# Optimization experiments

Hardware: AMD Instinct MI355X
Metric: run time of the kernel (lower is better)

The kernel has to match this reference:

```python
import jax, jax.numpy as jnp
import numpy as np

B, S, E, H, D, R = 2, 2048, 1024, 16, 64, 16


def setup_inputs() -> dict:
    key = jax.random.key(0)
    ks = jax.random.split(key, 9)
    s = lambda k, shape, fan: jax.random.normal(k, shape, dtype=jnp.float32) / np.sqrt(fan)
    return {
        "x": jax.random.normal(ks[0], (B, S, E), dtype=jnp.float32),
        "Wq": s(ks[1], (H, E, D), E),
        "bq": jnp.zeros((H, D), jnp.float32),
        "Wk": s(ks[2], (H, E, D), E),
        "bk": jnp.zeros((H, D), jnp.float32),
        "Wvd": s(ks[3], (H, E, R), E),
        "bvd": jnp.zeros((H, R), jnp.float32),
        "Wvu": s(ks[4], (H, R, D), R),
        "bvu": jnp.zeros((H, D), jnp.float32),
    }


def reference(x, Wq, bq, Wk, bk, Wvd, bvd, Wvu, bvu):
    b, s, e = x.shape
    # per-head projections, vectorized over heads h
    q = jnp.einsum('bse,hed->bhsd', x, Wq) + bq[None, :, None, :]
    k = jnp.einsum('bse,hed->bhsd', x, Wk) + bk[None, :, None, :]
    # NOTE: original scales by sqrt(embedding_dimension), not head dim
    scores = jnp.einsum('bhsd,bhtd->bhst', q, k) / jnp.sqrt(jnp.float32(e))
    # original mask: masked_fill where key_idx < query_idx (anti-causal)
    qi = jnp.arange(s)[:, None]
    ki = jnp.arange(s)[None, :]
    scores = jnp.where(ki < qi, -jnp.inf, scores)
    att = jax.nn.softmax(scores, axis=-1)  # dropout p=0 (eval)
    # low-rank value: up(down(x))
    vd = jnp.einsum('bse,her->bhsr', x, Wvd) + bvd[None, :, None, :]
    v = jnp.einsum('bhsr,hrd->bhsd', vd, Wvu) + bvu[None, :, None, :]
    out = jnp.einsum('bhst,bhtd->bhsd', att, v)
    # concat heads along last dim (head order = stack order)
    return out.transpose(0, 2, 1, 3).reshape(b, s, -1)
```

## Files before the change

kernel.cpp:

```cpp
#include <hip/hip_runtime.h>
#include <stdint.h>

#define B_ 2
#define S_ 2048
#define E_ 1024
#define H_ 16
#define D_ 64
#define R_ 16

typedef short s16x8 __attribute__((ext_vector_type(8)));
typedef float f32x4 __attribute__((ext_vector_type(4)));

#define K1_ 0.045084220027780106f
#define K0_ -28.853900817779268f

__device__ __forceinline__ unsigned short f2bf(float f) {
  union { float f; unsigned u; } v; v.f = f;
  return (unsigned short)((v.u + 0x8000u) >> 16);
}

__device__ __forceinline__ void load_lds16(const void* g, void* l) {
  __builtin_amdgcn_global_load_lds(
      (__attribute__((address_space(1))) void*)(g),
      (__attribute__((address_space(3))) void*)(l), 16, 0, 0);
}

__global__ void k_prep(const float* __restrict__ x,
                       const float* __restrict__ Wq, const float* __restrict__ Wk,
                       const float* __restrict__ Wvd, const float* __restrict__ Wvu,
                       const float* __restrict__ bq, const float* __restrict__ bk,
                       const float* __restrict__ bvd, const float* __restrict__ bvu,
                       unsigned short* __restrict__ xb, unsigned short* __restrict__ Wt,
                       float* __restrict__ ball) {
  __shared__ float T[64][65];
  const int blk = blockIdx.x;
  const int t = threadIdx.x;
  if (blk < 4096) {
    int i = (blk * 256 + t) * 4;
    float4 v = *(const float4*)(x + i);
    ushort4 o;
    o.x = f2bf(v.x); o.y = f2bf(v.y); o.z = f2bf(v.z); o.w = f2bf(v.w);
    *(ushort4*)(xb + i) = o;
  } else if (blk < 4608) {
    const int bb = blk - 4096;
    const int which = bb >> 8;
    const int h = (bb >> 4) & 15;
    const int et = bb & 15;
    const float scl = which ? 1.f : K1_;
    const float* src = (which ? Wk : Wq) + (h * E_ + et * 64) * D_;
#pragma unroll
    for (int pr = 0; pr < 4; ++pr) {
      const int row = pr * 16 + (t >> 4);
      const int col = (t & 15) * 4;
      float4 v = *(const float4*)(src + row * 64 + col);
      T[row][col] = v.x; T[row][col + 1] = v.y; T[row][col + 2] = v.z; T[row][col + 3] = v.w;
    }
    __syncthreads();
#pragma unroll
    for (int pr = 0; pr < 4; ++pr) {
      const int d = pr * 16 + (t >> 4);
      const int ec = (t & 15) * 4;
      ushort4 o;
      o.x = f2bf(T[ec][d] * scl); o.y = f2bf(T[ec + 1][d] * scl);
      o.z = f2bf(T[ec + 2][d] * scl); o.w = f2bf(T[ec + 3][d] * scl);
      *(ushort4*)(Wt + ((which << 10) + h * 64 + d) * 1024 + et * 64 + ec) = o;
    }
  } else if (blk < 8704) {
    const int idx = (blk - 4608) * 256 + t;
    const int row = idx >> 10;
    const int e = idx & 1023;
    const int h = row >> 6, d = row & 63;
    const float4* wd4 = (const float4*)(Wvd + (h << 14) + e * 16);
    const float* wu = Wvu + h * R_ * D_ + d;
    float acc = 0.f;
#pragma unroll
    for (int r4 = 0; r4 < 4; ++r4) {
      float4 a = wd4[r4];
      acc += a.x * wu[(r4 * 4 + 0) * 64];
      acc += a.y * wu[(r4 * 4 + 1) * 64];
      acc += a.z * wu[(r4 * 4 + 2) * 64];
      acc += a.w * wu[(r4 * 4 + 3) * 64];
    }
    Wt[(2048 + row) * 1024 + e] = f2bf(acc);
  } else {
    int n = (blk - 8704) * 256 + t;
    int which = n >> 10;
    int hd = n & 1023;
    int h = hd >> 6, d = hd & 63;
    float v;
    if (which == 0) v = bq[hd] * K1_;
    else if (which == 1) v = bk[hd];
    else {
      v = bvu[hd];
#pragma unroll
      for (int r = 0; r < R_; ++r) v += bvd[h * R_ + r] * Wvu[(h * R_ + r) * D_ + d];
    }
    ball[n] = v;
  }
}


__global__ __launch_bounds__(256, 2) void k_gemm_qkv(
    const unsigned short* __restrict__ X, const unsigned short* __restrict__ Wt,
    const float* __restrict__ ball,
    unsigned short* __restrict__ Qb, unsigned short* __restrict__ Kb,
    unsigned short* __restrict__ Vb) {
  __shared__ unsigned short As[128 * 32];
  __shared__ unsigned short Bs[128 * 32];
  const int tid = threadIdx.x;
  const int lane = tid & 63, wave = tid >> 6;
  const int quad = lane >> 4, l16 = lane & 15;
  const int mBase = blockIdx.y * 128, nBase = blockIdx.x * 128;
  const int wm = (wave & 1) * 64, wn = (wave >> 1) * 64;
  const int lrow = lane >> 2, lcol = (lane & 3) * 8;

  f32x4 acc[4][4];
#pragma unroll
  for (int mi = 0; mi < 4; ++mi)
#pragma unroll
    for (int ni = 0; ni < 4; ++ni) acc[mi][ni] = (f32x4){0.f, 0.f, 0.f, 0.f};

  for (int k0 = 0; k0 < E_; k0 += 32) {
#pragma unroll
    for (int i = 0; i < 2; ++i) {
      const int r0 = __builtin_amdgcn_readfirstlane((wave + i * 4) * 16);
      load_lds16(X + (mBase + r0 + lrow) * E_ + k0 + lcol, &As[r0 * 32]);
      load_lds16(Wt + (nBase + r0 + lrow) * E_ + k0 + lcol, &Bs[r0 * 32]);
    }
    __syncthreads();
    s16x8 af[4], bfr[4];
#pragma unroll
    for (int mi = 0; mi < 4; ++mi)
      af[mi] = *(const s16x8*)&As[(wm + mi * 16 + l16) * 32 + quad * 8];
#pragma unroll
    for (int ni = 0; ni < 4; ++ni)
      bfr[ni] = *(const s16x8*)&Bs[(wn + ni * 16 + l16) * 32 + quad * 8];
#pragma unroll
    for (int mi = 0; mi < 4; ++mi)
#pragma unroll
      for (int ni = 0; ni < 4; ++ni)
        acc[mi][ni] = __builtin_amdgcn_mfma_f32_16x16x32_bf16(af[mi], bfr[ni], acc[mi][ni], 0, 0, 0);
    __syncthreads();
  }

  const int which = nBase >> 10;
#pragma unroll
  for (int ni = 0; ni < 4; ++ni) {
    const int n = nBase + wn + ni * 16 + l16;
    const int nh = n & 1023;
    const int h = nh >> 6, d = nh & 63;
    const float bias = ball[n];
#pragma unroll
    for (int mi = 0; mi < 4; ++mi) {
      const int m0 = mBase + wm + mi * 16 + quad * 4;
      const int b = m0 >> 11;
      const int s = m0 & 2047;
      const int bh = b * H_ + h;
      if (which == 2) {
        ushort4 pk;
        pk.x = f2bf(acc[mi][ni][0] + bias);
        pk.y = f2bf(acc[mi][ni][1] + bias);
        pk.z = f2bf(acc[mi][ni][2] + bias);
        pk.w = f2bf(acc[mi][ni][3] + bias);
        *(ushort4*)(Vb + (bh * D_ + d) * S_ + s) = pk;
      } else {
        unsigned short* dst = (which == 0 ? Qb : Kb) + (bh * S_ + s) * D_ + d;
#pragma unroll
        for (int r = 0; r < 4; ++r) dst[r * D_] = f2bf(acc[mi][ni][r] + bias);
      }
    }
  }
}


__global__ __launch_bounds__(256, 4) void k_attn(
    const unsigned short* __restrict__ Qb, const unsigned short* __restrict__ Kb,
    const unsigned short* __restrict__ Vb, float* __restrict__ out) {
  __shared__ unsigned short Ks[2][2 * 64 * 32];
  __shared__ unsigned short Vs[2][2 * 64 * 32];
  __shared__ unsigned short Ps[4][16][40];
  const int tid = threadIdx.x;
  const int lane = tid & 63, wave = tid >> 6;
  const int quad = lane >> 4, l16 = lane & 15;
  const int chunk = blockIdx.x >> 8;
  const int j = blockIdx.x & 255;
  int qt = j >> 3;
  if (chunk & 1) qt = 31 - qt;
  const int bh = (j & 7) + 8 * chunk;
  const int q0 = qt * 64;
  const int lrow = lane >> 2, lcol = (lane & 3) * 8;
  const int r0 = __builtin_amdgcn_readfirstlane(wave * 16);
  const f32x4 kvec = {K0_, K0_, K0_, K0_};

  s16x8 qf[2];
  {
    const unsigned short* qp = Qb + (bh * S_ + q0 + wave * 16 + l16) * D_ + quad * 8;
    qf[0] = *(const s16x8*)qp;
    qf[1] = *(const s16x8*)(qp + 32);
  }
  f32x4 o[4];
#pragma unroll
  for (int dc = 0; dc < 4; ++dc) o[dc] = (f32x4){0.f, 0.f, 0.f, 0.f};
  float l_acc[4] = {0.f, 0.f, 0.f, 0.f};

#define DMA_KV(kt_, b_)                                                          \
  {                                                                              \
    _Pragma("unroll")                                                            \
    for (int hdc = 0; hdc < 2; ++hdc) {                                          \
      load_lds16(Kb + (bh * S_ + (kt_) * 64 + r0 + lrow) * D_ + hdc * 32 + lcol, \
                 &Ks[b_][hdc * 2048 + r0 * 32]);                                 \
      load_lds16(Vb + (bh * D_ + r0 + lrow) * S_ + (kt_) * 64 + hdc * 32 + lcol, \
                 &Vs[b_][hdc * 2048 + r0 * 32]);                                 \
    }                                                                            \
  }

  DMA_KV(qt, 0);

  int buf = 0;
  for (int kt = qt; kt < S_ / 64; ++kt) {
    __syncthreads();
    if (kt + 1 < S_ / 64) DMA_KV(kt + 1, buf ^ 1);

    const bool diag = (kt == qt);
#pragma unroll
    for (int kc = 0; kc < 2; ++kc) {
#pragma unroll
      for (int tcc = 0; tcc < 2; ++tcc) {
        const int tc = kc * 2 + tcc;
        f32x4 a = __builtin_amdgcn_mfma_f32_16x16x32_bf16(
            qf[0], *(const s16x8*)&Ks[buf][(tc * 16 + l16) * 32 + quad * 8], kvec, 0, 0, 0);
        f32x4 sc = __builtin_amdgcn_mfma_f32_16x16x32_bf16(
            qf[1], *(const s16x8*)&Ks[buf][2048 + (tc * 16 + l16) * 32 + quad * 8], a, 0, 0, 0);
        if (diag) {
#pragma unroll
          for (int r = 0; r < 4; ++r) {
            const int t = tc * 16 + l16;
            const int q = wave * 16 + quad * 4 + r;
            if (t < q) sc[r] = -200.f;
          }
        }
#pragma unroll
        for (int r = 0; r < 4; ++r) {
          float p = exp2f(sc[r]);
          l_acc[r] += p;
          Ps[wave][quad * 4 + r][tcc * 16 + l16] =
              (unsigned short)(__float_as_uint(p) >> 16);
        }
      }
      s16x8 pf = *(const s16x8*)&Ps[wave][l16][quad * 8];
#pragma unroll
      for (int dc = 0; dc < 4; ++dc) {
        s16x8 vb = *(const s16x8*)&Vs[buf][kc * 2048 + (dc * 16 + l16) * 32 + quad * 8];
        o[dc] = __builtin_amdgcn_mfma_f32_16x16x32_bf16(pf, vb, o[dc], 0, 0, 0);
      }
    }
    buf ^= 1;
  }
#undef DMA_KV

#pragma unroll
  for (int off = 1; off < 16; off <<= 1)
#pragma unroll
    for (int r = 0; r < 4; ++r) l_acc[r] += __shfl_xor(l_acc[r], off);
  float rinv[4];
#pragma unroll
  for (int r = 0; r < 4; ++r) rinv[r] = 1.f / l_acc[r];

  const int b = bh >> 4, h = bh & 15;
#pragma unroll
  for (int dc = 0; dc < 4; ++dc)
#pragma unroll
    for (int r = 0; r < 4; ++r) {
      const int s = q0 + wave * 16 + quad * 4 + r;
      out[(b * S_ + s) * (H_ * D_) + h * D_ + dc * 16 + l16] = o[dc][r] * rinv[r];
    }
}


extern "C" void kernel_launch(void* const* d_in, const int* in_sizes, int n_in,
                              void* d_out, int out_size, void* d_ws, size_t ws_size,
                              hipStream_t stream) {
  const float* x   = (const float*)d_in[0];
  const float* Wq  = (const float*)d_in[1];
  const float* bq  = (const float*)d_in[2];
  const float* Wk  = (const float*)d_in[3];
  const float* bk  = (const float*)d_in[4];
  const float* Wvd = (const float*)d_in[5];
  const float* bvd = (const float*)d_in[6];
  const float* Wvu = (const float*)d_in[7];
  const float* bvu = (const float*)d_in[8];
  float* out = (float*)d_out;

  char* ws = (char*)d_ws;
  unsigned short* xb   = (unsigned short*)(ws);
  unsigned short* Wt   = (unsigned short*)(ws + (8u << 20));
  float*          ball = (float*)(ws + (14u << 20));
  unsigned short* Qb   = (unsigned short*)(ws + (15u << 20));
  unsigned short* Kb   = (unsigned short*)(ws + (23u << 20));
  unsigned short* Vb   = (unsigned short*)(ws + (31u << 20));

  k_prep<<<8716, 256, 0, stream>>>(x, Wq, Wk, Wvd, Wvu, bq, bk, bvd, bvu, xb, Wt, ball);
  k_gemm_qkv<<<dim3(3072 / 128, 4096 / 128), 256, 0, stream>>>(xb, Wt, ball, Qb, Kb, Vb);
  k_attn<<<1024, 256, 0, stream>>>(Qb, Kb, Vb, out);
}
```

Baseline: 170.2 us.

## Balance anti-causal attention work with split-KV segments and combine kernel

Replaces the per-query-tile attention kernel with a load-balanced version: the 528 (q-tile, k-tile) pairs per head are split evenly across 32 blocks (16 or 17 steps each), and each block writes partial unnormalized outputs and row sums per segment. A new combine kernel sums the partials and normalizes. It also applies an XOR swizzle to the LDS layout of K/V to reduce bank conflicts. The cost is extra global traffic for the partials, a second kernel launch, and a dependence on enough workspace; otherwise it falls back to the old kernel.

```diff
diff --git a/kernel.cpp b/kernel.cpp
--- a/kernel.cpp
+++ b/kernel.cpp
@@ -99,7 +99,6 @@
   }
 }
 
-
 __global__ __launch_bounds__(256, 2) void k_gemm_qkv(
     const unsigned short* __restrict__ X, const unsigned short* __restrict__ Wt,
     const float* __restrict__ ball,
@@ -172,8 +171,177 @@
   }
 }
 
-
-__global__ __launch_bounds__(256, 4) void k_attn(
+__global__ __launch_bounds__(256, 4) void k_attn_bal(
+    const unsigned short* __restrict__ Qb, const unsigned short* __restrict__ Kb,
+    const unsigned short* __restrict__ Vb,
+    float* __restrict__ opart, float* __restrict__ lpart) {
+  __shared__ unsigned short Ks[2][2 * 64 * 32];
+  __shared__ unsigned short Vs[2][2 * 64 * 32];
+  __shared__ unsigned short Ps[4][16][40];
+  const int tid = threadIdx.x;
+  const int lane = tid & 63, wave = tid >> 6;
+  const int quad = lane >> 4, l16 = lane & 15;
+  const int blk = blockIdx.x;
+  const int bh = (blk & 7) + 8 * (blk >> 8);
+  const int w = (blk & 255) >> 3;
+  const int lo = (w < 16) ? 17 * w : 272 + 16 * (w - 16);
+  const int nsteps = (w < 16) ? 17 : 16;
+  const int r0 = __builtin_amdgcn_readfirstlane(wave * 16);
+  const f32x4 kvec = {K0_, K0_, K0_, K0_};
+
+  const int lrow = lane >> 2;
+  const int q3w  = ((lrow & 1) << 2) | (lane & 3);
+  const int q3e  = q3w ^ ((lrow >> 1) & 7);
+  const int sr16 = (lrow & ~1) | (q3e >> 2);
+  const int sc   = (q3e & 3) * 8;
+  const int rbase = (l16 >> 1) * 64 + ((((l16 & 1) << 2) | quad) ^ ((l16 >> 1) & 7)) * 8;
+
+  int qt = 0, uq = 0;
+  while (uq + (32 - qt) <= lo) { uq += 32 - qt; ++qt; }
+  int kt = qt + (lo - uq);
+
+  s16x8 qf0, qf1;
+  {
+    const unsigned short* qp = Qb + (bh * S_ + qt * 64 + wave * 16 + l16) * D_ + quad * 8;
+    qf0 = *(const s16x8*)qp; qf1 = *(const s16x8*)(qp + 32);
+  }
+  f32x4 o[4];
+#pragma unroll
+  for (int dc = 0; dc < 4; ++dc) o[dc] = (f32x4){0.f, 0.f, 0.f, 0.f};
+  float l_acc[4] = {0.f, 0.f, 0.f, 0.f};
+
+#define DMA_KV_B(kt_, b_)                                                         \
+  {                                                                               \
+    _Pragma("unroll")                                                             \
+    for (int hdc = 0; hdc < 2; ++hdc) {                                           \
+      load_lds16(Kb + (bh * S_ + (kt_) * 64 + r0 + sr16) * D_ + hdc * 32 + sc,    \
+                 &Ks[b_][hdc * 2048 + r0 * 32]);                                  \
+      load_lds16(Vb + (bh * D_ + r0 + sr16) * S_ + (kt_) * 64 + hdc * 32 + sc,    \
+                 &Vs[b_][hdc * 2048 + r0 * 32]);                                  \
+    }                                                                             \
+  }
+
+  DMA_KV_B(kt, 0);
+  int buf = 0;
+  int qt_n = qt, kt_n = kt;
+
+  for (int step = 0; step < nsteps; ++step) {
+    __syncthreads();
+    if (step + 1 < nsteps) {
+      if (kt_n < 31) ++kt_n; else { ++qt_n; kt_n = qt_n; }
+      DMA_KV_B(kt_n, buf ^ 1);
+    }
+
+    const bool diag = (kt == qt);
+#pragma unroll
+    for (int kc = 0; kc < 2; ++kc) {
+#pragma unroll
+      for (int tcc = 0; tcc < 2; ++tcc) {
+        const int tc = kc * 2 + tcc;
+        f32x4 a = __builtin_amdgcn_mfma_f32_16x16x32_bf16(
+            qf0, *(const s16x8*)&Ks[buf][tc * 512 + rbase], kvec, 0, 0, 0);
+        f32x4 sc4 = __builtin_amdgcn_mfma_f32_16x16x32_bf16(
+            qf1, *(const s16x8*)&Ks[buf][2048 + tc * 512 + rbase], a, 0, 0, 0);
+        if (diag) {
+#pragma unroll
+          for (int r = 0; r < 4; ++r) {
+            const int t = tc * 16 + l16;
+            const int q = wave * 16 + quad * 4 + r;
+            if (t < q) sc4[r] = -200.f;
+          }
+        }
+#pragma unroll
+        for (int r = 0; r < 4; ++r) {
+          float p = exp2f(sc4[r]);
+          l_acc[r] += p;
+          Ps[wave][quad * 4 + r][tcc * 16 + l16] =
+              (unsigned short)(__float_as_uint(p) >> 16);
+        }
+      }
+      s16x8 pf = *(const s16x8*)&Ps[wave][l16][quad * 8];
+#pragma unroll
+      for (int dc = 0; dc < 4; ++dc) {
+        s16x8 vb = *(const s16x8*)&Vs[buf][kc * 2048 + dc * 512 + rbase];
+        o[dc] = __builtin_amdgcn_mfma_f32_16x16x32_bf16(pf, vb, o[dc], 0, 0, 0);
+      }
+    }
+    buf ^= 1;
+
+    const bool segend = (kt == 31) || (step == nsteps - 1);
+    if (segend) {
+      float lr[4];
+#pragma unroll
+      for (int r = 0; r < 4; ++r) {
+        float v = l_acc[r];
+        v += __shfl_xor(v, 1); v += __shfl_xor(v, 2);
+        v += __shfl_xor(v, 4); v += __shfl_xor(v, 8);
+        lr[r] = v;
+      }
+      const int sidx = (uq < 272) ? (uq / 17) : 16 + ((uq - 272) >> 4);
+      const int slot = w - sidx;
+      const int pb = (bh * 32 + qt) * 3 + slot;
+      float* op = opart + pb * 4096 + (wave * 16) * 64;
+#pragma unroll
+      for (int dc = 0; dc < 4; ++dc)
+#pragma unroll
+        for (int r = 0; r < 4; ++r)
+          op[(quad * 4 + r) * 64 + dc * 16 + l16] = o[dc][r];
+      if (l16 == 0) {
+#pragma unroll
+        for (int r = 0; r < 4; ++r)
+          lpart[pb * 64 + wave * 16 + quad * 4 + r] = lr[r];
+      }
+      if (step + 1 < nsteps) {
+        uq += 32 - qt;
+        qt = qt_n;
+        const unsigned short* qp =
+            Qb + (bh * S_ + qt * 64 + wave * 16 + l16) * D_ + quad * 8;
+        qf0 = *(const s16x8*)qp; qf1 = *(const s16x8*)(qp + 32);
+#pragma unroll
+        for (int dc = 0; dc < 4; ++dc) o[dc] = (f32x4){0.f, 0.f, 0.f, 0.f};
+#pragma unroll
+        for (int r = 0; r < 4; ++r) l_acc[r] = 0.f;
+      }
+    }
+    kt = kt_n;
+  }
+#undef DMA_KV_B
+}
+
+__global__ void k_comb(const float* __restrict__ opart, const float* __restrict__ lpart,
+                       float* __restrict__ out) {
+  const int bh = blockIdx.x >> 5, qt = blockIdx.x & 31;
+  const int off = 32 * qt - (qt * (qt - 1)) / 2;
+  const int last = off + (32 - qt) - 1;
+  const int s0 = (off < 272) ? off / 17 : 16 + (off - 272) / 16;
+  const int s1 = (last < 272) ? last / 17 : 16 + (last - 272) / 16;
+  const int n = s1 - s0 + 1;
+  const int t = threadIdx.x;
+  const int row = t >> 2, d0 = (t & 3) * 16;
+  const int base = (bh * 32 + qt) * 3;
+  float l = 0.f;
+  f32x4 acc[4];
+#pragma unroll
+  for (int j = 0; j < 4; ++j) acc[j] = (f32x4){0.f, 0.f, 0.f, 0.f};
+  for (int s = 0; s < n; ++s) {
+    l += lpart[(base + s) * 64 + row];
+    const f32x4* op = (const f32x4*)(opart + (base + s) * 4096 + row * 64 + d0);
+#pragma unroll
+    for (int j = 0; j < 4; ++j) acc[j] += op[j];
+  }
+  const float rinv = 1.f / l;
+  const int b = bh >> 4, h = bh & 15;
+  float4* dst = (float4*)(out + (b * S_ + qt * 64 + row) * (H_ * D_) + h * D_ + d0);
+#pragma unroll
+  for (int j = 0; j < 4; ++j) {
+    float4 v;
+    v.x = acc[j][0] * rinv; v.y = acc[j][1] * rinv;
+    v.z = acc[j][2] * rinv; v.w = acc[j][3] * rinv;
+    dst[j] = v;
+  }
+}
+
+__global__ __launch_bounds__(256, 4) void k_attn_r0(
     const unsigned short* __restrict__ Qb, const unsigned short* __restrict__ Kb,
     const unsigned short* __restrict__ Vb, float* __restrict__ out) {
   __shared__ unsigned short Ks[2][2 * 64 * 32];
@@ -203,7 +371,7 @@
   for (int dc = 0; dc < 4; ++dc) o[dc] = (f32x4){0.f, 0.f, 0.f, 0.f};
   float l_acc[4] = {0.f, 0.f, 0.f, 0.f};
 
-#define DMA_KV(kt_, b_)                                                          \
+#define DMA_KV_R(kt_, b_)                                                        \
   {                                                                              \
     _Pragma("unroll")                                                            \
     for (int hdc = 0; hdc < 2; ++hdc) {                                          \
@@ -214,12 +382,12 @@
     }                                                                            \
   }
 
-  DMA_KV(qt, 0);
+  DMA_KV_R(qt, 0);
 
   int buf = 0;
   for (int kt = qt; kt < S_ / 64; ++kt) {
     __syncthreads();
-    if (kt + 1 < S_ / 64) DMA_KV(kt + 1, buf ^ 1);
+    if (kt + 1 < S_ / 64) DMA_KV_R(kt + 1, buf ^ 1);
 
     const bool diag = (kt == qt);
 #pragma unroll
@@ -256,7 +424,7 @@
     }
     buf ^= 1;
   }
-#undef DMA_KV
+#undef DMA_KV_R
 
 #pragma unroll
   for (int off = 1; off < 16; off <<= 1)
@@ -299,7 +467,21 @@
   unsigned short* Kb   = (unsigned short*)(ws + (23u << 20));
   unsigned short* Vb   = (unsigned short*)(ws + (31u << 20));
 
+  const size_t OPART_OFF = (size_t)40u << 20;
+  const size_t OPART_SZ  = (size_t)32 * 32 * 3 * 4096 * 4;
+  const size_t LPART_OFF = OPART_OFF + OPART_SZ;
+  const size_t LPART_SZ  = (size_t)32 * 32 * 3 * 64 * 4;
+  const size_t NEED      = LPART_OFF + LPART_SZ;
+
   k_prep<<<8716, 256, 0, stream>>>(x, Wq, Wk, Wvd, Wvu, bq, bk, bvd, bvu, xb, Wt, ball);
   k_gemm_qkv<<<dim3(3072 / 128, 4096 / 128), 256, 0, stream>>>(xb, Wt, ball, Qb, Kb, Vb);
-  k_attn<<<1024, 256, 0, stream>>>(Qb, Kb, Vb, out);
-}
+
+  if (ws_size >= NEED) {
+    float* opart = (float*)(ws + OPART_OFF);
+    float* lpart = (float*)(ws + LPART_OFF);
+    k_attn_bal<<<1024, 256, 0, stream>>>(Qb, Kb, Vb, opart, lpart);
+    k_comb<<<1024, 256, 0, stream>>>(opart, lpart, out);
+  } else {
+    k_attn_r0<<<1024, 256, 0, stream>>>(Qb, Kb, Vb, out);
+  }
+}
```

After: 184.2 us. 8.2% more time.

## Compute low-rank V via rank-16 down projection plus separate up-projection kernel

Applied to the files above, without the earlier changes.

Stops folding Wvd·Wvu into a full 1024x1024 V weight. The QKV GEMM now computes only the rank-16 down-projection, 256 columns instead of 1024, which cuts GEMM work by a quarter. A new k_vup kernel expands vd to the transposed V layout with bias. This adds a launch, an extra round trip through the vd buffer, and a second bf16 rounding of the intermediate.

```diff
diff --git a/kernel.cpp b/kernel.cpp
--- a/kernel.cpp
+++ b/kernel.cpp
@@ -18,6 +18,10 @@
   union { float f; unsigned u; } v; v.f = f;
   return (unsigned short)((v.u + 0x8000u) >> 16);
 }
+__device__ __forceinline__ float bf2f(unsigned short b) {
+  union { unsigned u; float f; } v; v.u = ((unsigned)b) << 16;
+  return v.f;
+}
 
 __device__ __forceinline__ void load_lds16(const void* g, void* l) {
   __builtin_amdgcn_global_load_lds(
@@ -27,9 +31,9 @@
 
 __global__ void k_prep(const float* __restrict__ x,
                        const float* __restrict__ Wq, const float* __restrict__ Wk,
-                       const float* __restrict__ Wvd, const float* __restrict__ Wvu,
+                       const float* __restrict__ Wvd,
                        const float* __restrict__ bq, const float* __restrict__ bk,
-                       const float* __restrict__ bvd, const float* __restrict__ bvu,
+                       const float* __restrict__ bvd,
                        unsigned short* __restrict__ xb, unsigned short* __restrict__ Wt,
                        float* __restrict__ ball) {
   __shared__ float T[64][65];
@@ -65,46 +69,32 @@
       o.z = f2bf(T[ec + 2][d] * scl); o.w = f2bf(T[ec + 3][d] * scl);
       *(ushort4*)(Wt + ((which << 10) + h * 64 + d) * 1024 + et * 64 + ec) = o;
     }
-  } else if (blk < 8704) {
-    const int idx = (blk - 4608) * 256 + t;
-    const int row = idx >> 10;
-    const int e = idx & 1023;
-    const int h = row >> 6, d = row & 63;
-    const float4* wd4 = (const float4*)(Wvd + (h << 14) + e * 16);
-    const float* wu = Wvu + h * R_ * D_ + d;
-    float acc = 0.f;
-#pragma unroll
-    for (int r4 = 0; r4 < 4; ++r4) {
-      float4 a = wd4[r4];
-      acc += a.x * wu[(r4 * 4 + 0) * 64];
-      acc += a.y * wu[(r4 * 4 + 1) * 64];
-      acc += a.z * wu[(r4 * 4 + 2) * 64];
-      acc += a.w * wu[(r4 * 4 + 3) * 64];
-    }
-    Wt[(2048 + row) * 1024 + e] = f2bf(acc);
+  } else if (blk < 4864) {
+    const int bb = blk - 4608;
+    const int h = bb >> 4, r = bb & 15;
+    const int e0 = t * 4;
+    const float* src = Wvd + (h << 14) + r;
+    ushort4 o;
+    o.x = f2bf(src[(e0 + 0) * 16]);
+    o.y = f2bf(src[(e0 + 1) * 16]);
+    o.z = f2bf(src[(e0 + 2) * 16]);
+    o.w = f2bf(src[(e0 + 3) * 16]);
+    *(ushort4*)(Wt + (2048 + bb) * 1024 + e0) = o;
   } else {
-    int n = (blk - 8704) * 256 + t;
+    int n = (blk - 4864) * 256 + t;
     int which = n >> 10;
     int hd = n & 1023;
-    int h = hd >> 6, d = hd & 63;
-    float v;
-    if (which == 0) v = bq[hd] * K1_;
-    else if (which == 1) v = bk[hd];
-    else {
-      v = bvu[hd];
-#pragma unroll
-      for (int r = 0; r < R_; ++r) v += bvd[h * R_ + r] * Wvu[(h * R_ + r) * D_ + d];
-    }
-    ball[n] = v;
-  }
-}
-
+    if (which == 0) ball[n] = bq[hd] * K1_;
+    else if (which == 1) ball[n] = bk[hd];
+    else if (hd < 256) ball[2048 + hd] = bvd[hd];
+  }
+}
 
 __global__ __launch_bounds__(256, 2) void k_gemm_qkv(
     const unsigned short* __restrict__ X, const unsigned short* __restrict__ Wt,
     const float* __restrict__ ball,
     unsigned short* __restrict__ Qb, unsigned short* __restrict__ Kb,
-    unsigned short* __restrict__ Vb) {
+    unsigned short* __restrict__ vd) {
   __shared__ unsigned short As[128 * 32];
   __shared__ unsigned short Bs[128 * 32];
   const int tid = threadIdx.x;
@@ -148,30 +138,62 @@
   for (int ni = 0; ni < 4; ++ni) {
     const int n = nBase + wn + ni * 16 + l16;
     const int nh = n & 1023;
-    const int h = nh >> 6, d = nh & 63;
     const float bias = ball[n];
 #pragma unroll
     for (int mi = 0; mi < 4; ++mi) {
       const int m0 = mBase + wm + mi * 16 + quad * 4;
       const int b = m0 >> 11;
       const int s = m0 & 2047;
-      const int bh = b * H_ + h;
       if (which == 2) {
-        ushort4 pk;
-        pk.x = f2bf(acc[mi][ni][0] + bias);
-        pk.y = f2bf(acc[mi][ni][1] + bias);
-        pk.z = f2bf(acc[mi][ni][2] + bias);
-        pk.w = f2bf(acc[mi][ni][3] + bias);
-        *(ushort4*)(Vb + (bh * D_ + d) * S_ + s) = pk;
+        const int h = nh >> 4, r = nh & 15;
+        const int bh = b * H_ + h;
+        unsigned short* dst = vd + (bh * S_ + s) * 16 + r;
+#pragma unroll
+        for (int rr = 0; rr < 4; ++rr) dst[rr * 16] = f2bf(acc[mi][ni][rr] + bias);
       } else {
+        const int h = nh >> 6, d = nh & 63;
+        const int bh = b * H_ + h;
         unsigned short* dst = (which == 0 ? Qb : Kb) + (bh * S_ + s) * D_ + d;
 #pragma unroll
-        for (int r = 0; r < 4; ++r) dst[r * D_] = f2bf(acc[mi][ni][r] + bias);
+        for (int rr = 0; rr < 4; ++rr) dst[rr * D_] = f2bf(acc[mi][ni][rr] + bias);
       }
     }
   }
 }
 
+__global__ __launch_bounds__(256) void k_vup(
+    const unsigned short* __restrict__ vd, const float* __restrict__ Wvu,
+    const float* __restrict__ bvu, unsigned short* __restrict__ Vb) {
+  const int blk = blockIdx.x;
+  const int bh = blk >> 6, d = blk & 63;
+  const int h = bh & 15;
+  const int s0 = threadIdx.x * 8;
+  float wu[16];
+#pragma unroll
+  for (int r = 0; r < 16; ++r) wu[r] = Wvu[(h * 16 + r) * 64 + d];
+  const float bias = bvu[h * 64 + d];
+
+  float accv[8];
+#pragma unroll
+  for (int j = 0; j < 8; ++j) accv[j] = bias;
+  const s16x8* vp = (const s16x8*)(vd + (bh * S_ + s0) * 16);
+#pragma unroll
+  for (int j = 0; j < 8; ++j) {
+    s16x8 a = vp[j * 2];
+    s16x8 b = vp[j * 2 + 1];
+#pragma unroll
+    for (int r = 0; r < 8; ++r) {
+      accv[j] += bf2f((unsigned short)a[r]) * wu[r];
+      accv[j] += bf2f((unsigned short)b[r]) * wu[8 + r];
+    }
+  }
+  ushort4 o0, o1;
+  o0.x = f2bf(accv[0]); o0.y = f2bf(accv[1]); o0.z = f2bf(accv[2]); o0.w = f2bf(accv[3]);
+  o1.x = f2bf(accv[4]); o1.y = f2bf(accv[5]); o1.z = f2bf(accv[6]); o1.w = f2bf(accv[7]);
+  unsigned short* dst = Vb + (bh * D_ + d) * S_ + s0;
+  *(ushort4*)(dst) = o0;
+  *(ushort4*)(dst + 4) = o1;
+}
 
 __global__ __launch_bounds__(256, 4) void k_attn(
     const unsigned short* __restrict__ Qb, const unsigned short* __restrict__ Kb,
@@ -298,8 +320,10 @@
   unsigned short* Qb   = (unsigned short*)(ws + (15u << 20));
   unsigned short* Kb   = (unsigned short*)(ws + (23u << 20));
   unsigned short* Vb   = (unsigned short*)(ws + (31u << 20));
-
-  k_prep<<<8716, 256, 0, stream>>>(x, Wq, Wk, Wvd, Wvu, bq, bk, bvd, bvu, xb, Wt, ball);
-  k_gemm_qkv<<<dim3(3072 / 128, 4096 / 128), 256, 0, stream>>>(xb, Wt, ball, Qb, Kb, Vb);
+  unsigned short* vd   = (unsigned short*)(ws + (39u << 20));
+
+  k_prep<<<4876, 256, 0, stream>>>(x, Wq, Wk, Wvd, bq, bk, bvd, xb, Wt, ball);
+  k_gemm_qkv<<<dim3(2304 / 128, 4096 / 128), 256, 0, stream>>>(xb, Wt, ball, Qb, Kb, vd);
+  k_vup<<<2048, 256, 0, stream>>>(vd, Wvu, bvu, Vb);
   k_attn<<<1024, 256, 0, stream>>>(Qb, Kb, Vb, out);
 }
```

Measured after the change: 183.5 us. 1.08x slower.
